# Kernel optimization log

Hardware: AMD Instinct MI355X
Metric: run time of the kernel (lower is better)

Reference implementation:

```python
import jax, jax.numpy as jnp
import numpy as np

B, S, D, H = 2, 2048, 1024, 16
HD = D // H

def setup_inputs() -> dict:
    key = jax.random.key(0)
    ks = jax.random.split(key, 11)
    s = 1.0 / np.sqrt(D)
    return {
        "query": jax.random.normal(ks[0], (B, S, D), jnp.float32),
        "key": jax.random.normal(ks[1], (B, S, D), jnp.float32),
        "value": jax.random.normal(ks[2], (B, S, D), jnp.float32),
        "Wq": jax.random.normal(ks[3], (D, D), jnp.float32) * s,
        "bq": jax.random.normal(ks[4], (D,), jnp.float32) * s,
        "Wk": jax.random.normal(ks[5], (D, D), jnp.float32) * s,
        "bk": jax.random.normal(ks[6], (D,), jnp.float32) * s,
        "Wv": jax.random.normal(ks[7], (D, D), jnp.float32) * s,
        "bv": jax.random.normal(ks[8], (D,), jnp.float32) * s,
        "Wo": jax.random.normal(ks[9], (D, D), jnp.float32) * s,
        "bo": jax.random.normal(ks[10], (D,), jnp.float32) * s,
        "test": 0,
    }

def _heads(x, W, b):
    # [B,S,D] @ [D,D] -> [B,S,D] -> [B,H,S,HD]
    y = x @ W + b
    return y.reshape(B, -1, H, HD).transpose(0, 2, 1, 3)

def reference(query, key, value, Wq, bq, Wk, bk, Wv, bv, Wo, bo, test):
    q = _heads(query, Wq, bq)
    k = _heads(key, Wk, bk)
    v = _heads(value, Wv, bv)
    scale = 1.0 / np.sqrt(HD).astype(np.float32)
    scores = jnp.einsum('bhqd,bhkd->bhqk', q, k) * scale  # [B,H,S,S]
    if test:
        return scores
    prob = jax.nn.softmax(scores, axis=-1)
    out = jnp.einsum('bhqk,bhkd->bhqd', prob, v)
    out = out.transpose(0, 2, 1, 3).reshape(B, -1, D)
    return out @ Wo + bo
```

## Files before the change

### kernel.cpp

```cpp
#include <hip/hip_runtime.h>

constexpr int Bn  = 2;
constexpr int Sn  = 2048;
constexpr int Dn  = 1024;
constexpr int Hn  = 16;
constexpr int HDn = 64;
constexpr int Mn  = Bn * Sn;

typedef _Float16 half8 __attribute__((ext_vector_type(8)));
typedef _Float16 half4 __attribute__((ext_vector_type(4)));
typedef float    f32x4 __attribute__((ext_vector_type(4)));

__device__ __forceinline__ void cp16(const _Float16* g, _Float16* l) {
  __builtin_amdgcn_global_load_lds(
      (__attribute__((address_space(1))) void*)g,
      (__attribute__((address_space(3))) void*)l, 16, 0, 0);
}

__global__ __launch_bounds__(256) void prep_kernel(
    const float* __restrict__ q, const float* __restrict__ k,
    const float* __restrict__ v,
    const float* __restrict__ Wq, const float* __restrict__ Wk,
    const float* __restrict__ Wv, const float* __restrict__ Wo,
    _Float16* __restrict__ Xh, _Float16* __restrict__ WT) {
  __shared__ float tile[64][65];
  const int n = blockIdx.x;
  const int tid = threadIdx.x;
  if (n < 12288) {
    const int z = n >> 12;
    const float* src = (z == 0) ? q : (z == 1) ? k : v;
    _Float16* dst = Xh + (size_t)z * (Mn * Dn);
    int i = (n & 4095) * 256 + tid;
    float4 v4 = ((const float4*)src)[i];
    half4 h;
    h.x = (_Float16)v4.x; h.y = (_Float16)v4.y;
    h.z = (_Float16)v4.z; h.w = (_Float16)v4.w;
    *(half4*)(dst + (size_t)i * 4) = h;
  } else {
    const int m = n - 12288;
    const int z = m >> 8, rem = m & 255;
    const float* W = (z == 0) ? Wq : (z == 1) ? Wk : (z == 2) ? Wv : Wo;
    _Float16* T = WT + (size_t)z * Dn * Dn;
    const int k0 = (rem >> 4) * 64, n0 = (rem & 15) * 64;
#pragma unroll
    for (int i = 0; i < 4; i++) {
      int s = tid + i * 256;
      int r = s >> 4, c4 = s & 15;
      float4 w4 = *(const float4*)(W + (size_t)(k0 + r) * Dn + n0 + c4 * 4);
      tile[r][c4 * 4 + 0] = w4.x; tile[r][c4 * 4 + 1] = w4.y;
      tile[r][c4 * 4 + 2] = w4.z; tile[r][c4 * 4 + 3] = w4.w;
    }
    __syncthreads();
#pragma unroll
    for (int i = 0; i < 2; i++) {
      int s = tid + i * 256;
      int nn = s >> 3, r8 = (s & 7) * 8;
      half8 h;
#pragma unroll
      for (int j = 0; j < 8; j++) h[j] = (_Float16)tile[r8 + j][nn];
      *(half8*)(T + (size_t)(n0 + nn) * Dn + k0 + r8) = h;
    }
  }
}

__global__ __launch_bounds__(256) void proj_kernel(
    const _Float16* __restrict__ Xh, const _Float16* __restrict__ WT,
    const float* __restrict__ bq, const float* __restrict__ bk,
    const float* __restrict__ bv,
    _Float16* __restrict__ Qh, _Float16* __restrict__ Kh,
    _Float16* __restrict__ VT) {
  const int z = blockIdx.z;
  const _Float16* A  = Xh + (size_t)z * Mn * Dn;
  const _Float16* Bm = WT + (size_t)z * Dn * Dn;
  const float* bias = (z == 0) ? bq : (z == 1) ? bk : bv;

  __shared__ __align__(16) _Float16 As[128 * 64];
  __shared__ __align__(16) _Float16 Bs[128 * 64];

  const int tid  = threadIdx.x;
  const int lane = tid & 63;
  const int w    = tid >> 6;
  const int wm   = (w >> 1) * 64;
  const int wn   = (w & 1) * 64;
  const int m0   = blockIdx.y * 128;
  const int n0   = blockIdx.x * 128;
  const int qd   = lane >> 4;
  const int lm   = lane & 15;

  const int st_r = tid >> 3;
  const int st_u = (tid & 7) ^ (st_r & 7);

  f32x4 acc[4][4];
#pragma unroll
  for (int i = 0; i < 4; i++)
#pragma unroll
    for (int j = 0; j < 4; j++) acc[i][j] = {0.f, 0.f, 0.f, 0.f};

  for (int k0 = 0; k0 < Dn; k0 += 64) {
#pragma unroll
    for (int p = 0; p < 4; p++) {
      int row = st_r + p * 32;
      cp16(A + (size_t)(m0 + row) * Dn + k0 + st_u * 8, As + (tid + p * 256) * 8);
      cp16(Bm + (size_t)(n0 + row) * Dn + k0 + st_u * 8, Bs + (tid + p * 256) * 8);
    }
    __syncthreads();
#pragma unroll
    for (int ks = 0; ks < 2; ks++) {
      const int up = ((ks * 4 + qd) ^ (lm & 7)) * 8;
      half8 a[4], bb[4];
#pragma unroll
      for (int mi = 0; mi < 4; mi++)
        a[mi] = *(const half8*)(As + (wm + mi * 16 + lm) * 64 + up);
#pragma unroll
      for (int ni = 0; ni < 4; ni++)
        bb[ni] = *(const half8*)(Bs + (wn + ni * 16 + lm) * 64 + up);
      if (z < 2) {
#pragma unroll
        for (int mi = 0; mi < 4; mi++)
#pragma unroll
          for (int ni = 0; ni < 4; ni++)
            acc[mi][ni] = __builtin_amdgcn_mfma_f32_16x16x32_f16(bb[ni], a[mi], acc[mi][ni], 0, 0, 0);
      } else {
#pragma unroll
        for (int mi = 0; mi < 4; mi++)
#pragma unroll
          for (int ni = 0; ni < 4; ni++)
            acc[mi][ni] = __builtin_amdgcn_mfma_f32_16x16x32_f16(a[mi], bb[ni], acc[mi][ni], 0, 0, 0);
      }
    }
    __syncthreads();
  }

  if (z < 2) {
    _Float16* out = (z == 0) ? Qh : Kh;
    const float scl = (z == 0) ? 0.125f * 1.44269504089f : 1.0f;
#pragma unroll
    for (int mi = 0; mi < 4; mi++) {
      int m = m0 + wm + mi * 16 + lm;
      int b_ = m >> 11, s_ = m & (Sn - 1);
#pragma unroll
      for (int ni = 0; ni < 4; ni++) {
        int nb = n0 + wn + ni * 16 + qd * 4;
        float4 b4 = *(const float4*)(bias + nb);
        int h = nb >> 6, hd = nb & 63;
        half4 h4;
        h4[0] = (_Float16)((acc[mi][ni][0] + b4.x) * scl);
        h4[1] = (_Float16)((acc[mi][ni][1] + b4.y) * scl);
        h4[2] = (_Float16)((acc[mi][ni][2] + b4.z) * scl);
        h4[3] = (_Float16)((acc[mi][ni][3] + b4.w) * scl);
        *(half4*)(out + (((size_t)(b_ * Hn + h)) * Sn + s_) * HDn + hd) = h4;
      }
    }
  } else {
#pragma unroll
    for (int ni = 0; ni < 4; ni++) {
      int n = n0 + wn + ni * 16 + lm;
      float b_f = bias[n];
      int h = n >> 6, hd = n & 63;
#pragma unroll
      for (int mi = 0; mi < 4; mi++) {
        int mb = m0 + wm + mi * 16 + qd * 4;
        int b_ = mb >> 11, s_ = mb & (Sn - 1);
        half4 h4;
#pragma unroll
        for (int r = 0; r < 4; r++) h4[r] = (_Float16)(acc[mi][ni][r] + b_f);
        *(half4*)(VT + (((size_t)(b_ * Hn + h)) * HDn + hd) * Sn + s_) = h4;
      }
    }
  }
}

__global__ __launch_bounds__(256, 3) void attn_kernel(
    const _Float16* __restrict__ Qh, const _Float16* __restrict__ Kh,
    const _Float16* __restrict__ VT, _Float16* __restrict__ attn_out) {
  constexpr int PV_LD = 72;
  __shared__ __align__(16) _Float16 Ksb[2][128 * 64];
  __shared__ __align__(16) _Float16 Ps[4 * 32 * PV_LD];

  const int n    = blockIdx.x;
  const int slot = n >> 3;
  const int bh   = (n & 7) * 4 + (slot >> 4);
  const int q0   = (slot & 15) * 128;
  const size_t base = (size_t)bh * Sn * HDn;

  const int tid  = threadIdx.x;
  const int lane = tid & 63;
  const int w    = tid >> 6;
  const int qd   = lane >> 4;
  const int lm   = lane & 15;

  const _Float16* qptr = Qh + base + (size_t)(q0 + w * 32 + lm) * HDn + qd * 8;
  half8 qa[2][2];
#pragma unroll
  for (int nj = 0; nj < 2; nj++)
#pragma unroll
    for (int ks = 0; ks < 2; ks++)
      qa[nj][ks] = *(const half8*)(qptr + nj * 16 * HDn + ks * 32);

  half8 vones;
#pragma unroll
  for (int j = 0; j < 8; j++) vones[j] = (lm == 0) ? (_Float16)1.0f : (_Float16)0.0f;

  f32x4 oacc[2][4];
#pragma unroll
  for (int i = 0; i < 2; i++)
#pragma unroll
    for (int j = 0; j < 4; j++) oacc[i][j] = {0.f, 0.f, 0.f, 0.f};
  f32x4 oaccl[2] = {{0.f, 0.f, 0.f, 0.f}, {0.f, 0.f, 0.f, 0.f}};

  _Float16* Psw = Ps + w * (32 * PV_LD);
  const f32x4 sinit = {-10.f, -10.f, -10.f, -10.f};

  const int st_r = tid >> 3;
  const int st_u = (tid & 7) ^ (st_r & 7);
  const _Float16* kbase = Kh + base;

#define STAGE_K(KT, DST)                                                     \
  {                                                                          \
    const _Float16* src_ = kbase + (size_t)(KT) * 128 * HDn;                 \
    _Float16* dst_ = (DST);                                                  \
    _Pragma("unroll")                                                        \
    for (int p = 0; p < 4; p++)                                              \
      cp16(src_ + (size_t)(st_r + p * 32) * HDn + st_u * 8,                  \
           dst_ + (tid + p * 256) * 8);                                      \
  }

  STAGE_K(0, Ksb[0])
  __syncthreads();

  int cur = 0;
  for (int kt = 0; kt < Sn / 128; kt++) {
    const int kb = kt * 128;
    if (kt + 1 < Sn / 128) STAGE_K(kt + 1, Ksb[cur ^ 1])

#pragma unroll
    for (int c = 0; c < 2; c++) {
      f32x4 sacc[4][2];
#pragma unroll
      for (int n4 = 0; n4 < 4; n4++)
#pragma unroll
        for (int nj = 0; nj < 2; nj++) sacc[n4][nj] = sinit;
#pragma unroll
      for (int n4 = 0; n4 < 4; n4++) {
        int ni = 4 * c + n4;
#pragma unroll
        for (int ks = 0; ks < 2; ks++) {
          int up = (4 * ks + qd) ^ (lm & 7);
          half8 ka = *(const half8*)(Ksb[cur] + (ni * 16 + lm) * HDn + up * 8);
#pragma unroll
          for (int nj = 0; nj < 2; nj++)
            sacc[n4][nj] = __builtin_amdgcn_mfma_f32_16x16x32_f16(ka, qa[nj][ks], sacc[n4][nj], 0, 0, 0);
        }
      }

      half8 vb[4][2];
#pragma unroll
      for (int oi = 0; oi < 4; oi++)
#pragma unroll
        for (int k2 = 0; k2 < 2; k2++)
          vb[oi][k2] = *(const half8*)(VT + base + (size_t)(oi * 16 + lm) * Sn
                                       + kb + c * 64 + k2 * 32 + qd * 8);

#pragma unroll
      for (int nj = 0; nj < 2; nj++)
#pragma unroll
        for (int n4 = 0; n4 < 4; n4++) {
          float p0 = __builtin_amdgcn_exp2f(sacc[n4][nj][0]);
          float p1 = __builtin_amdgcn_exp2f(sacc[n4][nj][1]);
          float p2 = __builtin_amdgcn_exp2f(sacc[n4][nj][2]);
          float p3 = __builtin_amdgcn_exp2f(sacc[n4][nj][3]);
          auto lo = __builtin_amdgcn_cvt_pkrtz(p0, p1);
          auto hi = __builtin_amdgcn_cvt_pkrtz(p2, p3);
          half4 h4;
          h4[0] = (_Float16)lo[0]; h4[1] = (_Float16)lo[1];
          h4[2] = (_Float16)hi[0]; h4[3] = (_Float16)hi[1];
          *(half4*)(Psw + (nj * 16 + lm) * PV_LD + n4 * 16 + qd * 4) = h4;
        }

#pragma unroll
      for (int k2 = 0; k2 < 2; k2++) {
        half8 pa[2];
#pragma unroll
        for (int mi = 0; mi < 2; mi++)
          pa[mi] = *(const half8*)(Psw + (mi * 16 + lm) * PV_LD + k2 * 32 + qd * 8);
#pragma unroll
        for (int oi = 0; oi < 4; oi++)
#pragma unroll
          for (int mi = 0; mi < 2; mi++)
            oacc[mi][oi] = __builtin_amdgcn_mfma_f32_16x16x32_f16(vb[oi][k2], pa[mi], oacc[mi][oi], 0, 0, 0);
#pragma unroll
        for (int mi = 0; mi < 2; mi++)
          oaccl[mi] = __builtin_amdgcn_mfma_f32_16x16x32_f16(vones, pa[mi], oaccl[mi], 0, 0, 0);
      }
    }

    __syncthreads();
    cur ^= 1;
  }
#undef STAGE_K

  const int b_ = bh >> 4, h_ = bh & 15;
#pragma unroll
  for (int mi = 0; mi < 2; mi++) {
    float lr = __shfl(oaccl[mi][0], lm, 64);
    float inv = 1.0f / lr;
    int qrow = q0 + w * 32 + mi * 16 + lm;
    size_t rowbase = ((size_t)(b_ * Sn + qrow)) * Dn + h_ * 64;
#pragma unroll
    for (int oi = 0; oi < 4; oi++) {
      half4 h4;
#pragma unroll
      for (int r = 0; r < 4; r++) h4[r] = (_Float16)(oacc[mi][oi][r] * inv);
      *(half4*)(attn_out + rowbase + oi * 16 + qd * 4) = h4;
    }
  }
}

__global__ __launch_bounds__(256) void outproj_kernel(
    const _Float16* __restrict__ Aattn, const _Float16* __restrict__ WoT,
    const float* __restrict__ bo, float* __restrict__ out) {
  __shared__ __align__(16) _Float16 As[64 * 64];
  __shared__ __align__(16) _Float16 Bs[128 * 64];

  const int tid  = threadIdx.x;
  const int lane = tid & 63;
  const int w    = tid >> 6;
  const int wm   = (w >> 1) * 32;
  const int wn   = (w & 1) * 64;
  const int m0   = blockIdx.y * 64;
  const int n0   = blockIdx.x * 128;
  const int qd   = lane >> 4;
  const int lm   = lane & 15;

  const int st_r = tid >> 3;
  const int st_u = (tid & 7) ^ (st_r & 7);

  f32x4 acc[2][4];
#pragma unroll
  for (int i = 0; i < 2; i++)
#pragma unroll
    for (int j = 0; j < 4; j++) acc[i][j] = {0.f, 0.f, 0.f, 0.f};

  for (int k0 = 0; k0 < Dn; k0 += 64) {
#pragma unroll
    for (int p = 0; p < 2; p++) {
      int row = st_r + p * 32;
      cp16(Aattn + (size_t)(m0 + row) * Dn + k0 + st_u * 8, As + (tid + p * 256) * 8);
    }
#pragma unroll
    for (int p = 0; p < 4; p++) {
      int row = st_r + p * 32;
      cp16(WoT + (size_t)(n0 + row) * Dn + k0 + st_u * 8, Bs + (tid + p * 256) * 8);
    }
    __syncthreads();
#pragma unroll
    for (int ks = 0; ks < 2; ks++) {
      const int up = ((ks * 4 + qd) ^ (lm & 7)) * 8;
      half8 a[2], bb[4];
#pragma unroll
      for (int mi = 0; mi < 2; mi++)
        a[mi] = *(const half8*)(As + (wm + mi * 16 + lm) * 64 + up);
#pragma unroll
      for (int ni = 0; ni < 4; ni++)
        bb[ni] = *(const half8*)(Bs + (wn + ni * 16 + lm) * 64 + up);
#pragma unroll
      for (int mi = 0; mi < 2; mi++)
#pragma unroll
        for (int ni = 0; ni < 4; ni++)
          acc[mi][ni] = __builtin_amdgcn_mfma_f32_16x16x32_f16(bb[ni], a[mi], acc[mi][ni], 0, 0, 0);
    }
    __syncthreads();
  }
#pragma unroll
  for (int mi = 0; mi < 2; mi++) {
    int m = m0 + wm + mi * 16 + lm;
#pragma unroll
    for (int ni = 0; ni < 4; ni++) {
      int nb = n0 + wn + ni * 16 + qd * 4;
      float4 b4 = *(const float4*)(bo + nb);
      float4 o4;
      o4.x = acc[mi][ni][0] + b4.x;
      o4.y = acc[mi][ni][1] + b4.y;
      o4.z = acc[mi][ni][2] + b4.z;
      o4.w = acc[mi][ni][3] + b4.w;
      *(float4*)(out + (size_t)m * Dn + nb) = o4;
    }
  }
}

extern "C" void kernel_launch(void* const* d_in, const int* in_sizes, int n_in,
                              void* d_out, int out_size, void* d_ws, size_t ws_size,
                              hipStream_t stream) {
  const float* query = (const float*)d_in[0];
  const float* key_  = (const float*)d_in[1];
  const float* value = (const float*)d_in[2];
  const float* Wq = (const float*)d_in[3];
  const float* bq = (const float*)d_in[4];
  const float* Wk = (const float*)d_in[5];
  const float* bk = (const float*)d_in[6];
  const float* Wv = (const float*)d_in[7];
  const float* bv = (const float*)d_in[8];
  const float* Wo = (const float*)d_in[9];
  const float* bo = (const float*)d_in[10];

  _Float16* Xh = (_Float16*)d_ws;
  _Float16* WT = Xh + (size_t)3 * Mn * Dn;
  _Float16* Qh = WT + (size_t)4 * Dn * Dn;
  _Float16* Kh = Qh + (size_t)Mn * Dn;
  _Float16* VT = Kh + (size_t)Mn * Dn;
  _Float16* attnb = Xh;
  float* out = (float*)d_out;

  dim3 blk(256);
  prep_kernel<<<dim3(12288 + 1024), blk, 0, stream>>>(
      query, key_, value, Wq, Wk, Wv, Wo, Xh, WT);
  proj_kernel<<<dim3(Dn / 128, Mn / 128, 3), blk, 0, stream>>>(
      Xh, WT, bq, bk, bv, Qh, Kh, VT);
  attn_kernel<<<dim3(512), blk, 0, stream>>>(Qh, Kh, VT, attnb);
  outproj_kernel<<<dim3(Dn / 128, Mn / 64), blk, 0, stream>>>(
      attnb, WT + (size_t)3 * Dn * Dn, bo, out);
}
```

Baseline: 254.6 us.

## Halve attention query tile to 64 rows and double grid size

```diff
diff --git a/kernel.cpp b/kernel.cpp
--- a/kernel.cpp
+++ b/kernel.cpp
@@ -170,17 +170,16 @@
   }
 }
 
-__global__ __launch_bounds__(256, 3) void attn_kernel(
+__global__ __launch_bounds__(256, 4) void attn_kernel(
     const _Float16* __restrict__ Qh, const _Float16* __restrict__ Kh,
     const _Float16* __restrict__ VT, _Float16* __restrict__ attn_out) {
-  constexpr int PV_LD = 72;
   __shared__ __align__(16) _Float16 Ksb[2][128 * 64];
-  __shared__ __align__(16) _Float16 Ps[4 * 32 * PV_LD];
+  __shared__ __align__(16) _Float16 Ps[4 * 16 * 64];
 
   const int n    = blockIdx.x;
   const int slot = n >> 3;
-  const int bh   = (n & 7) * 4 + (slot >> 4);
-  const int q0   = (slot & 15) * 128;
+  const int bh   = (n & 7) * 4 + (slot >> 5);
+  const int q0   = (slot & 31) * 64;
   const size_t base = (size_t)bh * Sn * HDn;
 
   const int tid  = threadIdx.x;
@@ -189,26 +188,23 @@
   const int qd   = lane >> 4;
   const int lm   = lane & 15;
 
-  const _Float16* qptr = Qh + base + (size_t)(q0 + w * 32 + lm) * HDn + qd * 8;
-  half8 qa[2][2];
-#pragma unroll
-  for (int nj = 0; nj < 2; nj++)
-#pragma unroll
-    for (int ks = 0; ks < 2; ks++)
-      qa[nj][ks] = *(const half8*)(qptr + nj * 16 * HDn + ks * 32);
+  const _Float16* qptr = Qh + base + (size_t)(q0 + w * 16 + lm) * HDn + qd * 8;
+  half8 qa[2];
+#pragma unroll
+  for (int ks = 0; ks < 2; ks++)
+    qa[ks] = *(const half8*)(qptr + ks * 32);
 
   half8 vones;
 #pragma unroll
   for (int j = 0; j < 8; j++) vones[j] = (lm == 0) ? (_Float16)1.0f : (_Float16)0.0f;
 
-  f32x4 oacc[2][4];
-#pragma unroll
-  for (int i = 0; i < 2; i++)
-#pragma unroll
-    for (int j = 0; j < 4; j++) oacc[i][j] = {0.f, 0.f, 0.f, 0.f};
-  f32x4 oaccl[2] = {{0.f, 0.f, 0.f, 0.f}, {0.f, 0.f, 0.f, 0.f}};
-
-  _Float16* Psw = Ps + w * (32 * PV_LD);
+  f32x4 oacc[4];
+#pragma unroll
+  for (int j = 0; j < 4; j++) oacc[j] = {0.f, 0.f, 0.f, 0.f};
+  f32x4 oaccl = {0.f, 0.f, 0.f, 0.f};
+
+  char* Psw = (char*)Ps + w * (16 * 64 * 2);
+  const int swz = (lm & 7) << 4;
   const f32x4 sinit = {-10.f, -10.f, -10.f, -10.f};
 
   const int st_r = tid >> 3;
@@ -235,11 +231,9 @@
 
 #pragma unroll
     for (int c = 0; c < 2; c++) {
-      f32x4 sacc[4][2];
-#pragma unroll
-      for (int n4 = 0; n4 < 4; n4++)
-#pragma unroll
-        for (int nj = 0; nj < 2; nj++) sacc[n4][nj] = sinit;
+      f32x4 sacc[4];
+#pragma unroll
+      for (int n4 = 0; n4 < 4; n4++) sacc[n4] = sinit;
 #pragma unroll
       for (int n4 = 0; n4 < 4; n4++) {
         int ni = 4 * c + n4;
@@ -247,9 +241,7 @@
         for (int ks = 0; ks < 2; ks++) {
           int up = (4 * ks + qd) ^ (lm & 7);
           half8 ka = *(const half8*)(Ksb[cur] + (ni * 16 + lm) * HDn + up * 8);
-#pragma unroll
-          for (int nj = 0; nj < 2; nj++)
-            sacc[n4][nj] = __builtin_amdgcn_mfma_f32_16x16x32_f16(ka, qa[nj][ks], sacc[n4][nj], 0, 0, 0);
+          sacc[n4] = __builtin_amdgcn_mfma_f32_16x16x32_f16(ka, qa[ks], sacc[n4], 0, 0, 0);
         }
       }
 
@@ -262,35 +254,26 @@
                                        + kb + c * 64 + k2 * 32 + qd * 8);
 
 #pragma unroll
-      for (int nj = 0; nj < 2; nj++)
-#pragma unroll
-        for (int n4 = 0; n4 < 4; n4++) {
-          float p0 = __builtin_amdgcn_exp2f(sacc[n4][nj][0]);
-          float p1 = __builtin_amdgcn_exp2f(sacc[n4][nj][1]);
-          float p2 = __builtin_amdgcn_exp2f(sacc[n4][nj][2]);
-          float p3 = __builtin_amdgcn_exp2f(sacc[n4][nj][3]);
-          auto lo = __builtin_amdgcn_cvt_pkrtz(p0, p1);
-          auto hi = __builtin_amdgcn_cvt_pkrtz(p2, p3);
-          half4 h4;
-          h4[0] = (_Float16)lo[0]; h4[1] = (_Float16)lo[1];
-          h4[2] = (_Float16)hi[0]; h4[3] = (_Float16)hi[1];
-          *(half4*)(Psw + (nj * 16 + lm) * PV_LD + n4 * 16 + qd * 4) = h4;
-        }
+      for (int n4 = 0; n4 < 4; n4++) {
+        float p0 = __builtin_amdgcn_exp2f(sacc[n4][0]);
+        float p1 = __builtin_amdgcn_exp2f(sacc[n4][1]);
+        float p2 = __builtin_amdgcn_exp2f(sacc[n4][2]);
+        float p3 = __builtin_amdgcn_exp2f(sacc[n4][3]);
+        auto lo = __builtin_amdgcn_cvt_pkrtz(p0, p1);
+        auto hi = __builtin_amdgcn_cvt_pkrtz(p2, p3);
+        half4 h4;
+        h4[0] = (_Float16)lo[0]; h4[1] = (_Float16)lo[1];
+        h4[2] = (_Float16)hi[0]; h4[3] = (_Float16)hi[1];
+        *(half4*)(Psw + lm * 128 + ((n4 * 32 + qd * 8) ^ swz)) = h4;
+      }
 
 #pragma unroll
       for (int k2 = 0; k2 < 2; k2++) {
-        half8 pa[2];
-#pragma unroll
-        for (int mi = 0; mi < 2; mi++)
-          pa[mi] = *(const half8*)(Psw + (mi * 16 + lm) * PV_LD + k2 * 32 + qd * 8);
+        half8 pa = *(const half8*)(Psw + lm * 128 + ((k2 * 64 + qd * 16) ^ swz));
 #pragma unroll
         for (int oi = 0; oi < 4; oi++)
-#pragma unroll
-          for (int mi = 0; mi < 2; mi++)
-            oacc[mi][oi] = __builtin_amdgcn_mfma_f32_16x16x32_f16(vb[oi][k2], pa[mi], oacc[mi][oi], 0, 0, 0);
-#pragma unroll
-        for (int mi = 0; mi < 2; mi++)
-          oaccl[mi] = __builtin_amdgcn_mfma_f32_16x16x32_f16(vones, pa[mi], oaccl[mi], 0, 0, 0);
+          oacc[oi] = __builtin_amdgcn_mfma_f32_16x16x32_f16(vb[oi][k2], pa, oacc[oi], 0, 0, 0);
+        oaccl = __builtin_amdgcn_mfma_f32_16x16x32_f16(vones, pa, oaccl, 0, 0, 0);
       }
     }
 
@@ -300,19 +283,16 @@
 #undef STAGE_K
 
   const int b_ = bh >> 4, h_ = bh & 15;
-#pragma unroll
-  for (int mi = 0; mi < 2; mi++) {
-    float lr = __shfl(oaccl[mi][0], lm, 64);
-    float inv = 1.0f / lr;
-    int qrow = q0 + w * 32 + mi * 16 + lm;
-    size_t rowbase = ((size_t)(b_ * Sn + qrow)) * Dn + h_ * 64;
-#pragma unroll
-    for (int oi = 0; oi < 4; oi++) {
-      half4 h4;
-#pragma unroll
-      for (int r = 0; r < 4; r++) h4[r] = (_Float16)(oacc[mi][oi][r] * inv);
-      *(half4*)(attn_out + rowbase + oi * 16 + qd * 4) = h4;
-    }
+  float lr = __shfl(oaccl[0], lm, 64);
+  float inv = 1.0f / lr;
+  int qrow = q0 + w * 16 + lm;
+  size_t rowbase = ((size_t)(b_ * Sn + qrow)) * Dn + h_ * 64;
+#pragma unroll
+  for (int oi = 0; oi < 4; oi++) {
+    half4 h4;
+#pragma unroll
+    for (int r = 0; r < 4; r++) h4[r] = (_Float16)(oacc[oi][r] * inv);
+    *(half4*)(attn_out + rowbase + oi * 16 + qd * 4) = h4;
   }
 }
 
@@ -416,7 +396,7 @@
       query, key_, value, Wq, Wk, Wv, Wo, Xh, WT);
   proj_kernel<<<dim3(Dn / 128, Mn / 128, 3), blk, 0, stream>>>(
       Xh, WT, bq, bk, bv, Qh, Kh, VT);
-  attn_kernel<<<dim3(512), blk, 0, stream>>>(Qh, Kh, VT, attnb);
+  attn_kernel<<<dim3(1024), blk, 0, stream>>>(Qh, Kh, VT, attnb);
   outproj_kernel<<<dim3(Dn / 128, Mn / 64), blk, 0, stream>>>(
       attnb, WT + (size_t)3 * Dn * Dn, bo, out);
 }
```

New measurement: 308.9 us. 1.21x slower.

## Feed softmax probabilities to PV MFMA directly from registers, drop LDS staging

Applied to the files above, without the earlier changes.

```diff
diff --git a/kernel.cpp b/kernel.cpp
--- a/kernel.cpp
+++ b/kernel.cpp
@@ -170,12 +170,10 @@
   }
 }
 
-__global__ __launch_bounds__(256, 3) void attn_kernel(
+__global__ __launch_bounds__(256) void attn_kernel(
     const _Float16* __restrict__ Qh, const _Float16* __restrict__ Kh,
     const _Float16* __restrict__ VT, _Float16* __restrict__ attn_out) {
-  constexpr int PV_LD = 72;
   __shared__ __align__(16) _Float16 Ksb[2][128 * 64];
-  __shared__ __align__(16) _Float16 Ps[4 * 32 * PV_LD];
 
   const int n    = blockIdx.x;
   const int slot = n >> 3;
@@ -197,9 +195,9 @@
     for (int ks = 0; ks < 2; ks++)
       qa[nj][ks] = *(const half8*)(qptr + nj * 16 * HDn + ks * 32);
 
-  half8 vones;
-#pragma unroll
-  for (int j = 0; j < 8; j++) vones[j] = (lm == 0) ? (_Float16)1.0f : (_Float16)0.0f;
+  half4 vones4;
+#pragma unroll
+  for (int j = 0; j < 4; j++) vones4[j] = (lm == 0) ? (_Float16)1.0f : (_Float16)0.0f;
 
   f32x4 oacc[2][4];
 #pragma unroll
@@ -208,12 +206,12 @@
     for (int j = 0; j < 4; j++) oacc[i][j] = {0.f, 0.f, 0.f, 0.f};
   f32x4 oaccl[2] = {{0.f, 0.f, 0.f, 0.f}, {0.f, 0.f, 0.f, 0.f}};
 
-  _Float16* Psw = Ps + w * (32 * PV_LD);
   const f32x4 sinit = {-10.f, -10.f, -10.f, -10.f};
 
   const int st_r = tid >> 3;
   const int st_u = (tid & 7) ^ (st_r & 7);
   const _Float16* kbase = Kh + base;
+  const _Float16* vrow  = VT + base + (size_t)lm * Sn + qd * 4;
 
 #define STAGE_K(KT, DST)                                                     \
   {                                                                          \
@@ -235,6 +233,14 @@
 
 #pragma unroll
     for (int c = 0; c < 2; c++) {
+      half4 va[4][4];
+#pragma unroll
+      for (int oi = 0; oi < 4; oi++)
+#pragma unroll
+        for (int n4 = 0; n4 < 4; n4++)
+          va[oi][n4] = *(const half4*)(vrow + (size_t)(oi * 16) * Sn
+                                       + kb + c * 64 + n4 * 16);
+
       f32x4 sacc[4][2];
 #pragma unroll
       for (int n4 = 0; n4 < 4; n4++)
@@ -252,14 +258,6 @@
             sacc[n4][nj] = __builtin_amdgcn_mfma_f32_16x16x32_f16(ka, qa[nj][ks], sacc[n4][nj], 0, 0, 0);
         }
       }
-
-      half8 vb[4][2];
-#pragma unroll
-      for (int oi = 0; oi < 4; oi++)
-#pragma unroll
-        for (int k2 = 0; k2 < 2; k2++)
-          vb[oi][k2] = *(const half8*)(VT + base + (size_t)(oi * 16 + lm) * Sn
-                                       + kb + c * 64 + k2 * 32 + qd * 8);
 
 #pragma unroll
       for (int nj = 0; nj < 2; nj++)
@@ -271,27 +269,14 @@
           float p3 = __builtin_amdgcn_exp2f(sacc[n4][nj][3]);
           auto lo = __builtin_amdgcn_cvt_pkrtz(p0, p1);
           auto hi = __builtin_amdgcn_cvt_pkrtz(p2, p3);
-          half4 h4;
-          h4[0] = (_Float16)lo[0]; h4[1] = (_Float16)lo[1];
-          h4[2] = (_Float16)hi[0]; h4[3] = (_Float16)hi[1];
-          *(half4*)(Psw + (nj * 16 + lm) * PV_LD + n4 * 16 + qd * 4) = h4;
+          half4 pb;
+          pb[0] = (_Float16)lo[0]; pb[1] = (_Float16)lo[1];
+          pb[2] = (_Float16)hi[0]; pb[3] = (_Float16)hi[1];
+#pragma unroll
+          for (int oi = 0; oi < 4; oi++)
+            oacc[nj][oi] = __builtin_amdgcn_mfma_f32_16x16x16f16(va[oi][n4], pb, oacc[nj][oi], 0, 0, 0);
+          oaccl[nj] = __builtin_amdgcn_mfma_f32_16x16x16f16(vones4, pb, oaccl[nj], 0, 0, 0);
         }
-
-#pragma unroll
-      for (int k2 = 0; k2 < 2; k2++) {
-        half8 pa[2];
-#pragma unroll
-        for (int mi = 0; mi < 2; mi++)
-          pa[mi] = *(const half8*)(Psw + (mi * 16 + lm) * PV_LD + k2 * 32 + qd * 8);
-#pragma unroll
-        for (int oi = 0; oi < 4; oi++)
-#pragma unroll
-          for (int mi = 0; mi < 2; mi++)
-            oacc[mi][oi] = __builtin_amdgcn_mfma_f32_16x16x32_f16(vb[oi][k2], pa[mi], oacc[mi][oi], 0, 0, 0);
-#pragma unroll
-        for (int mi = 0; mi < 2; mi++)
-          oaccl[mi] = __builtin_amdgcn_mfma_f32_16x16x32_f16(vones, pa[mi], oaccl[mi], 0, 0, 0);
-      }
     }
 
     __syncthreads();
```

After: 304.8 us. 19.7% more time.
